# Kernel tuning notes

Hardware: AMD Instinct MI355X
Metric: run time of the kernel (lower is better)

Reference implementation:

```python
import jax, jax.numpy as jnp
import numpy as np

NUM_CHANNELS = 512
B_DIM = 64
C_DIM = 16
N = 512
FEAT = NUM_CHANNELS * 4 * 4  # 8192


def setup_inputs() -> dict:
    key = jax.random.key(0)
    k1, k2 = jax.random.split(key)
    inp = jax.random.normal(k1, (N, NUM_CHANNELS, 4, 4), dtype=jnp.float32)
    T = jax.random.normal(k2, (FEAT, B_DIM * C_DIM), dtype=jnp.float32) * 0.1
    return {"inp": inp, "T": T}


def reference(inp, T):
    x = inp.reshape(-1, FEAT)                      # (N, 8192)
    M = (x @ T).reshape(-1, B_DIM, C_DIM)          # (N, B, C)
    # pairwise L1 distance over C: (N, N, B)
    dist = jnp.sum(jnp.abs(M[:, None, :, :] - M[None, :, :, :]), axis=-1)
    o = jnp.sum(jnp.exp(-dist), axis=1)            # (N, B)
    return jnp.concatenate((x, o), axis=1)         # (N, 8192 + B)
```

## Files before the change

### kernel.cpp

```cpp
#include <hip/hip_runtime.h>

#define NROWS 512
#define FEAT  8192
#define BDIM  64
#define CDIM  16
#define MCOLS 1024
#define OUTC  8256
#define KSPLIT 8
#define KCHUNK (FEAT / KSPLIT)
#define KSTEPS (KCHUNK / 64)
#define MSIZE  (NROWS * MCOLS)

typedef __bf16 bf16x8 __attribute__((ext_vector_type(8)));
typedef float  floatx4 __attribute__((ext_vector_type(4)));

static __device__ __forceinline__ unsigned int pk2(float a, float b) {
    unsigned short lo = __builtin_bit_cast(unsigned short, (__bf16)a);
    unsigned short hi = __builtin_bit_cast(unsigned short, (__bf16)b);
    return (unsigned int)lo | ((unsigned int)hi << 16);
}

__global__ __launch_bounds__(512, 2) void k_gemm(const float* __restrict__ x,
                                                 const float* __restrict__ T,
                                                 float* __restrict__ Mp) {
    __shared__ __align__(16) unsigned short ldsA[2][128 * 64];
    __shared__ __align__(16) unsigned short ldsB[2][128 * 64];
    char* ldsAc = (char*)ldsA;
    char* ldsBc = (char*)ldsB;

    int bid = blockIdx.x;
    int wg = (bid & 7) * 32 + (bid >> 3);
    int mt = wg & 3, nt = (wg >> 2) & 7, ks = wg >> 5;
    int m0 = mt * 128, n0 = nt * 128, kbase = ks * KCHUNK;
    int t = threadIdx.x, w = t >> 6, l = t & 63;

    int arow = t >> 4, aq = t & 15;
    const float* gA = x + (size_t)(m0 + arow) * FEAT + kbase + aq * 4;
    int swa = (arow & 7) ^ ((arow >> 2) & 7);
    int wA = arow * 128 + (((aq >> 1) ^ swa) << 4) + ((aq & 1) << 3);

    int n4 = t & 31, kg = t >> 5;
    const float* gB = T + (size_t)(kbase + kg * 4) * MCOLS + n0 + n4 * 4;
    int wB[4];
#pragma unroll
    for (int j = 0; j < 4; ++j) {
        int n = n4 * 4 + j;
        int swn = (n & 7) ^ ((n >> 2) & 7);
        wB[j] = n * 128 + (((kg >> 1) ^ swn) << 4) + ((kg & 1) << 3);
    }

    int wr = w >> 2, wc = w & 3, fm = l & 15, fq = l >> 4;
    int swf = (fm & 7) ^ ((fm >> 2) & 7);
    int baseA = (wr * 64 + fm) * 128 + ((fq ^ swf) << 4);
    int baseB = (wc * 32 + fm) * 128 + ((fq ^ swf) << 4);

    floatx4 acc[4][2] = {};
    float4 va0[4], vb0[4], va1[4], vb1[4];

    auto issue = [&](int KK, float4* A4, float4* B4) {
        const float* pa = gA + KK * 64;
        A4[0] = *(const float4*)(pa);
        A4[1] = *(const float4*)(pa + 32 * FEAT);
        A4[2] = *(const float4*)(pa + 64 * FEAT);
        A4[3] = *(const float4*)(pa + 96 * FEAT);
        const float* pb = gB + (size_t)KK * 64 * MCOLS;
        B4[0] = *(const float4*)(pb);
        B4[1] = *(const float4*)(pb + MCOLS);
        B4[2] = *(const float4*)(pb + 2 * MCOLS);
        B4[3] = *(const float4*)(pb + 3 * MCOLS);
    };

    auto step = [&](int KK, int SO, float4* A4, float4* B4) {
#pragma unroll
        for (int r = 0; r < 4; ++r) {
            uint2 u; u.x = pk2(A4[r].x, A4[r].y); u.y = pk2(A4[r].z, A4[r].w);
            *(uint2*)(ldsAc + SO + wA + r * 4096) = u;
        }
        {
            uint2 u;
            u.x = pk2(B4[0].x, B4[1].x); u.y = pk2(B4[2].x, B4[3].x);
            *(uint2*)(ldsBc + SO + wB[0]) = u;
            u.x = pk2(B4[0].y, B4[1].y); u.y = pk2(B4[2].y, B4[3].y);
            *(uint2*)(ldsBc + SO + wB[1]) = u;
            u.x = pk2(B4[0].z, B4[1].z); u.y = pk2(B4[2].z, B4[3].z);
            *(uint2*)(ldsBc + SO + wB[2]) = u;
            u.x = pk2(B4[0].w, B4[1].w); u.y = pk2(B4[2].w, B4[3].w);
            *(uint2*)(ldsBc + SO + wB[3]) = u;
        }
        if (KK + 2 < KSTEPS) issue(KK + 2, A4, B4);
        asm volatile("s_waitcnt lgkmcnt(0)" ::: "memory");
        __builtin_amdgcn_s_barrier();
#pragma unroll
        for (int h = 0; h < 2; ++h) {
            bf16x8 af[4], bfr[2];
#pragma unroll
            for (int a = 0; a < 4; ++a)
                af[a] = *(const bf16x8*)(ldsAc + SO + ((baseA + a * 2048) ^ ((h ^ (a & 1)) << 6)));
#pragma unroll
            for (int b = 0; b < 2; ++b)
                bfr[b] = *(const bf16x8*)(ldsBc + SO + ((baseB + b * 2048) ^ ((h ^ (b & 1)) << 6)));
#pragma unroll
            for (int a = 0; a < 4; ++a)
#pragma unroll
                for (int b = 0; b < 2; ++b)
                    acc[a][b] = __builtin_amdgcn_mfma_f32_16x16x32_bf16(af[a], bfr[b], acc[a][b], 0, 0, 0);
        }
    };

    issue(0, va0, vb0);
    issue(1, va1, vb1);
    for (int kk = 0; kk < KSTEPS; kk += 2) {
        step(kk,     0,     va0, vb0);
        step(kk + 1, 16384, va1, vb1);
    }

    float* outp = Mp + (size_t)ks * MSIZE;
    int gr0 = m0 + wr * 64, gc0 = n0 + wc * 32;
#pragma unroll
    for (int a = 0; a < 4; ++a)
#pragma unroll
        for (int r = 0; r < 4; ++r) {
            int row = gr0 + a * 16 + fq * 4 + r;
#pragma unroll
            for (int b = 0; b < 2; ++b)
                outp[(size_t)row * MCOLS + gc0 + b * 16 + fm] = acc[a][b][r];
        }
}

__global__ __launch_bounds__(512, 2) void k_pair(const float* __restrict__ x,
                                                 const float* __restrict__ Mp,
                                                 float* __restrict__ out) {
    __shared__ float ldsM[NROWS * 20];
    __shared__ float partial[8][64];
    int bid = blockIdx.x, t = threadIdx.x;
    int b = bid & 63, itp = bid >> 6;

#pragma unroll
    for (int p = 0; p < 4; ++p) {
        int idx = t + p * 512;
        int j = idx >> 2, c4 = idx & 3;
        const float* base = Mp + (size_t)j * MCOLS + b * CDIM + c4 * 4;
        float4 s = *(const float4*)base;
#pragma unroll
        for (int k = 1; k < KSPLIT; ++k) {
            float4 v = *(const float4*)(base + (size_t)k * MSIZE);
            s.x += v.x; s.y += v.y; s.z += v.z; s.w += v.w;
        }
        *(float4*)&ldsM[j * 20 + c4 * 4] = s;
    }

    {
        const float* src = x + (size_t)bid * 2 * FEAT;
        float* dst = out + (size_t)bid * 2 * OUTC;
#pragma unroll
        for (int i = 0; i < 8; ++i) {
            int idx = t + i * 512;
            float4 v = *(const float4*)(src + (size_t)(idx >> 11) * FEAT + (idx & 2047) * 4);
            *(float4*)(dst + (size_t)(idx >> 11) * OUTC + (idx & 2047) * 4) = v;
        }
    }
    __syncthreads();

    int lane = t & 63, w = t >> 6, g = t >> 8, wg = (t >> 6) & 3;
    int i = (itp * 2 + g) * 64 + lane;
    float mi[CDIM];
#pragma unroll
    for (int cc = 0; cc < CDIM; ++cc) mi[cc] = ldsM[i * 20 + cc];

    float acc = 0.0f;
    for (int jj = wg * 128; jj < wg * 128 + 128; ++jj) {
        float d = 0.0f;
#pragma unroll
        for (int cc = 0; cc < CDIM; ++cc) d += fabsf(mi[cc] - ldsM[jj * 20 + cc]);
        acc += __expf(-d);
    }
    partial[w][lane] = acc;
    __syncthreads();
    if ((t & 255) < 64) {
        int ii = (itp * 2 + g) * 64 + (t & 63);
        float o = partial[g * 4 + 0][t & 63] + partial[g * 4 + 1][t & 63] +
                  partial[g * 4 + 2][t & 63] + partial[g * 4 + 3][t & 63];
        out[(size_t)ii * OUTC + FEAT + b] = o;
    }
}

extern "C" void kernel_launch(void* const* d_in, const int* in_sizes, int n_in,
                              void* d_out, int out_size, void* d_ws, size_t ws_size,
                              hipStream_t stream) {
    const float* x = (const float*)d_in[0];
    const float* T = (const float*)d_in[1];
    float* out = (float*)d_out;

    float* Mp = (float*)d_ws;

    k_gemm<<<256, 512, 0, stream>>>(x, T, Mp);
    k_pair<<<256, 512, 0, stream>>>(x, Mp, out);
}
```

Measured before the change: 130.3 us.

## Fuse input copy into GEMM loads and double split-K to 512 blocks

The x passthrough copy moves out of the pairwise kernel into the GEMM. One block per K-chunk writes the fp32 A-tile values it already loaded, so x is read once instead of twice. Split-K goes from 8 to 16, which doubles the block count to fill more CUs, and the loop drops to a single register prefetch stage so occupancy can reach 4 blocks. In exchange, the pair kernel must reduce twice as many partial M buffers, the GEMM writes twice the partial-sum traffic, and the shallower prefetch may expose more load latency.

```diff
diff --git a/kernel.cpp b/kernel.cpp
--- a/kernel.cpp
+++ b/kernel.cpp
@@ -6,7 +6,7 @@
 #define CDIM  16
 #define MCOLS 1024
 #define OUTC  8256
-#define KSPLIT 8
+#define KSPLIT 16
 #define KCHUNK (FEAT / KSPLIT)
 #define KSTEPS (KCHUNK / 64)
 #define MSIZE  (NROWS * MCOLS)
@@ -20,22 +20,25 @@
     return (unsigned int)lo | ((unsigned int)hi << 16);
 }
 
-__global__ __launch_bounds__(512, 2) void k_gemm(const float* __restrict__ x,
+__global__ __launch_bounds__(512, 4) void k_gemm(const float* __restrict__ x,
                                                  const float* __restrict__ T,
-                                                 float* __restrict__ Mp) {
+                                                 float* __restrict__ Mp,
+                                                 float* __restrict__ out) {
     __shared__ __align__(16) unsigned short ldsA[2][128 * 64];
     __shared__ __align__(16) unsigned short ldsB[2][128 * 64];
     char* ldsAc = (char*)ldsA;
     char* ldsBc = (char*)ldsB;
 
     int bid = blockIdx.x;
-    int wg = (bid & 7) * 32 + (bid >> 3);
+    int wg = (bid & 7) * 64 + (bid >> 3);
     int mt = wg & 3, nt = (wg >> 2) & 7, ks = wg >> 5;
     int m0 = mt * 128, n0 = nt * 128, kbase = ks * KCHUNK;
     int t = threadIdx.x, w = t >> 6, l = t & 63;
+    bool docopy = (nt == (ks & 7));
 
     int arow = t >> 4, aq = t & 15;
     const float* gA = x + (size_t)(m0 + arow) * FEAT + kbase + aq * 4;
+    float* gC = out + (size_t)(m0 + arow) * OUTC + kbase + aq * 4;
     int swa = (arow & 7) ^ ((arow >> 2) & 7);
     int wA = arow * 128 + (((aq >> 1) ^ swa) << 4) + ((aq & 1) << 3);
 
@@ -55,40 +58,48 @@
     int baseB = (wc * 32 + fm) * 128 + ((fq ^ swf) << 4);
 
     floatx4 acc[4][2] = {};
-    float4 va0[4], vb0[4], va1[4], vb1[4];
+    float4 va[4], vb[4];
 
-    auto issue = [&](int KK, float4* A4, float4* B4) {
+    auto issue = [&](int KK) {
         const float* pa = gA + KK * 64;
-        A4[0] = *(const float4*)(pa);
-        A4[1] = *(const float4*)(pa + 32 * FEAT);
-        A4[2] = *(const float4*)(pa + 64 * FEAT);
-        A4[3] = *(const float4*)(pa + 96 * FEAT);
+        va[0] = *(const float4*)(pa);
+        va[1] = *(const float4*)(pa + 32 * FEAT);
+        va[2] = *(const float4*)(pa + 64 * FEAT);
+        va[3] = *(const float4*)(pa + 96 * FEAT);
         const float* pb = gB + (size_t)KK * 64 * MCOLS;
-        B4[0] = *(const float4*)(pb);
-        B4[1] = *(const float4*)(pb + MCOLS);
-        B4[2] = *(const float4*)(pb + 2 * MCOLS);
-        B4[3] = *(const float4*)(pb + 3 * MCOLS);
+        vb[0] = *(const float4*)(pb);
+        vb[1] = *(const float4*)(pb + MCOLS);
+        vb[2] = *(const float4*)(pb + 2 * MCOLS);
+        vb[3] = *(const float4*)(pb + 3 * MCOLS);
     };
 
-    auto step = [&](int KK, int SO, float4* A4, float4* B4) {
+    issue(0);
+    for (int kk = 0; kk < KSTEPS; ++kk) {
+        int SO = (kk & 1) << 14;
 #pragma unroll
         for (int r = 0; r < 4; ++r) {
-            uint2 u; u.x = pk2(A4[r].x, A4[r].y); u.y = pk2(A4[r].z, A4[r].w);
+            uint2 u; u.x = pk2(va[r].x, va[r].y); u.y = pk2(va[r].z, va[r].w);
             *(uint2*)(ldsAc + SO + wA + r * 4096) = u;
         }
         {
             uint2 u;
-            u.x = pk2(B4[0].x, B4[1].x); u.y = pk2(B4[2].x, B4[3].x);
+            u.x = pk2(vb[0].x, vb[1].x); u.y = pk2(vb[2].x, vb[3].x);
             *(uint2*)(ldsBc + SO + wB[0]) = u;
-            u.x = pk2(B4[0].y, B4[1].y); u.y = pk2(B4[2].y, B4[3].y);
+            u.x = pk2(vb[0].y, vb[1].y); u.y = pk2(vb[2].y, vb[3].y);
             *(uint2*)(ldsBc + SO + wB[1]) = u;
-            u.x = pk2(B4[0].z, B4[1].z); u.y = pk2(B4[2].z, B4[3].z);
+            u.x = pk2(vb[0].z, vb[1].z); u.y = pk2(vb[2].z, vb[3].z);
             *(uint2*)(ldsBc + SO + wB[2]) = u;
-            u.x = pk2(B4[0].w, B4[1].w); u.y = pk2(B4[2].w, B4[3].w);
+            u.x = pk2(vb[0].w, vb[1].w); u.y = pk2(vb[2].w, vb[3].w);
             *(uint2*)(ldsBc + SO + wB[3]) = u;
         }
-        if (KK + 2 < KSTEPS) issue(KK + 2, A4, B4);
+        if (docopy) {
+#pragma unroll
+            for (int r = 0; r < 4; ++r)
+                *(float4*)(gC + (size_t)r * 32 * OUTC + kk * 64) = va[r];
+        }
+        if (kk + 1 < KSTEPS) issue(kk + 1);
         asm volatile("s_waitcnt lgkmcnt(0)" ::: "memory");
+        __builtin_amdgcn_sched_barrier(0);
         __builtin_amdgcn_s_barrier();
 #pragma unroll
         for (int h = 0; h < 2; ++h) {
@@ -105,13 +116,6 @@
                 for (int b = 0; b < 2; ++b)
                     acc[a][b] = __builtin_amdgcn_mfma_f32_16x16x32_bf16(af[a], bfr[b], acc[a][b], 0, 0, 0);
         }
-    };
-
-    issue(0, va0, vb0);
-    issue(1, va1, vb1);
-    for (int kk = 0; kk < KSTEPS; kk += 2) {
-        step(kk,     0,     va0, vb0);
-        step(kk + 1, 16384, va1, vb1);
     }
 
     float* outp = Mp + (size_t)ks * MSIZE;
@@ -127,8 +131,7 @@
         }
 }
 
-__global__ __launch_bounds__(512, 2) void k_pair(const float* __restrict__ x,
-                                                 const float* __restrict__ Mp,
+__global__ __launch_bounds__(512, 1) void k_pair(const float* __restrict__ Mp,
                                                  float* __restrict__ out) {
     __shared__ float ldsM[NROWS * 20];
     __shared__ float partial[8][64];
@@ -147,17 +150,6 @@
             s.x += v.x; s.y += v.y; s.z += v.z; s.w += v.w;
         }
         *(float4*)&ldsM[j * 20 + c4 * 4] = s;
-    }
-
-    {
-        const float* src = x + (size_t)bid * 2 * FEAT;
-        float* dst = out + (size_t)bid * 2 * OUTC;
-#pragma unroll
-        for (int i = 0; i < 8; ++i) {
-            int idx = t + i * 512;
-            float4 v = *(const float4*)(src + (size_t)(idx >> 11) * FEAT + (idx & 2047) * 4);
-            *(float4*)(dst + (size_t)(idx >> 11) * OUTC + (idx & 2047) * 4) = v;
-        }
     }
     __syncthreads();
 
@@ -193,6 +185,6 @@
 
     float* Mp = (float*)d_ws;
 
-    k_gemm<<<256, 512, 0, stream>>>(x, T, Mp);
-    k_pair<<<256, 512, 0, stream>>>(x, Mp, out);
+    k_gemm<<<512, 512, 0, stream>>>(x, T, Mp, out);
+    k_pair<<<256, 512, 0, stream>>>(Mp, out);
 }
```

Result: slower. 140.9 us (+8.2%).
